# Kernel optimization log

Measured on AMD Instinct MI355X. Metric: run time of the kernel, lower is better.

## Reference

```python
import jax, jax.numpy as jnp
import numpy as np

EPS = 1e-5

def group_norm(x, groups, w, b):
    # x: (B, C, ...) -> normalize over each group of channels + spatial dims
    B, C = x.shape[0], x.shape[1]
    xr = x.reshape(B, groups, -1)
    mu = xr.mean(-1, keepdims=True)
    var = xr.var(-1, keepdims=True)
    xn = ((xr - mu) * jax.lax.rsqrt(var + EPS)).reshape(x.shape)
    wshape = (1, C) + (1,) * (x.ndim - 2)
    return xn * w.reshape(wshape) + b.reshape(wshape)

def dwconv1d(x, w):
    # x: (B, Cg, L), w: (Cg, 1, k) depthwise, 'same' padding (odd k)
    k = w.shape[-1]
    return jax.lax.conv_general_dilated(
        x, w, window_strides=(1,), padding=[(k // 2, k // 2)],
        dimension_numbers=('NCH', 'OIH', 'NCH'),
        feature_group_count=x.shape[1])

def setup_inputs() -> dict:
    key = jax.random.key(0)
    ks = jax.random.split(key, 16)
    B, C, H, W = 32, 256, 56, 56
    Cg = C // 4
    inp = {'x': jax.random.normal(ks[0], (B, C, H, W), jnp.float32)}
    for i, k in enumerate((3, 5, 7, 9)):
        inp[f'dwh{i}'] = jax.random.normal(ks[1 + i], (Cg, 1, k), jnp.float32) * 0.2
        inp[f'dww{i}'] = jax.random.normal(ks[5 + i], (Cg, 1, k), jnp.float32) * 0.2
    inp['gnh_w'] = jnp.ones((C,), jnp.float32)
    inp['gnh_b'] = jnp.zeros((C,), jnp.float32)
    inp['gnw_w'] = jnp.ones((C,), jnp.float32)
    inp['gnw_b'] = jnp.zeros((C,), jnp.float32)
    inp['gn1_w'] = jnp.ones((C,), jnp.float32)
    inp['gn1_b'] = jnp.zeros((C,), jnp.float32)
    inp['wq'] = jax.random.normal(ks[13], (C,), jnp.float32)
    inp['wk'] = jax.random.normal(ks[14], (C,), jnp.float32)
    inp['wv'] = jax.random.normal(ks[15], (C,), jnp.float32)
    return inp

def reference(x, dwh0, dwh1, dwh2, dwh3, dww0, dww1, dww2, dww3,
              gnh_w, gnh_b, gnw_w, gnw_b, gn1_w, gn1_b, wq, wk, wv):
    B, C, H, W = x.shape
    n, Cg, p, gn_groups = 4, C // 4, 7, 4
    dwh = (dwh0, dwh1, dwh2, dwh3)
    dww = (dww0, dww1, dww2, dww3)

    # ---- SMSA: pooled multi-kernel depthwise 1D convs ----
    x_h = x.mean(axis=3)  # (B, C, H)
    x_w = x.mean(axis=2)  # (B, C, W)
    h_cat = jnp.concatenate(
        [dwconv1d(x_h[:, i * Cg:(i + 1) * Cg], dwh[i]) for i in range(n)], axis=1)
    w_cat = jnp.concatenate(
        [dwconv1d(x_w[:, i * Cg:(i + 1) * Cg], dww[i]) for i in range(n)], axis=1)
    Ah = jax.nn.sigmoid(group_norm(h_cat, gn_groups, gnh_w, gnh_b))  # (B,C,H)
    Aw = jax.nn.sigmoid(group_norm(w_cat, gn_groups, gnw_w, gnw_b))  # (B,C,W)
    x_s = x * (Ah[..., :, None] * Aw[..., None, :])  # (B,C,H,W)

    # ---- PCSA: adaptive pool to (p,p) then channel self-attention ----
    # H % p == 0 and W % p == 0, so adaptive avg pool == block mean
    xp = x_s.reshape(B, C, p, H // p, p, W // p).mean(axis=(3, 5))  # (B,C,p,p)
    xp = group_norm(xp, 1, gn1_w, gn1_b)
    N = p * p
    xf = xp.reshape(B, C, N)
    q = xf * wq[None, :, None]  # 1x1 depthwise conv == per-channel scale
    k = xf * wk[None, :, None]
    v = xf * wv[None, :, None]
    attn = jnp.einsum('bcn,bdn->bcd', q, k) / np.sqrt(float(N))
    attn = jax.nn.softmax(attn, axis=-1)
    o = jnp.einsum('bcd,bdn->bcn', attn, v)  # (B,C,N)
    Mc = jax.nn.sigmoid(o.mean(axis=-1))  # (B,C) adaptive avg pool to 1
    return x_s * Mc[:, :, None, None]
```

## Files before the change

kernel.cpp:

```cpp
#include <hip/hip_runtime.h>
#include <math.h>

#define B_  32
#define C_  256
#define H_  56
#define W_  56
#define CG_ 64
#define NG_ 4
#define P_  7
#define N_  49
#define XPP_ 52
#define PLP_ 57
#define PLANE_ (H_*W_)
#define NBC_ (B_*C_)
#define EPS_ 1e-5f

typedef float f4v __attribute__((ext_vector_type(4)));
typedef short s4v __attribute__((ext_vector_type(4)));
typedef short s8v __attribute__((ext_vector_type(8)));
typedef unsigned int uint32;

__device__ __forceinline__ float sig_(float v) { return 1.0f / (1.0f + expf(-v)); }

__device__ __forceinline__ short f2bf_(float f) {
  uint32 u = __builtin_bit_cast(uint32, f);
  u = (u + 0x7FFFu + ((u >> 16) & 1u)) >> 16;
  return (short)u;
}
__device__ __forceinline__ float bf2f_(short s) {
  uint32 u = ((uint32)(unsigned short)s) << 16;
  return __builtin_bit_cast(float, u);
}

__global__ __launch_bounds__(256) void k1_means_bf(const float* __restrict__ x,
                                                   float* __restrict__ xh,
                                                   float* __restrict__ xw,
                                                   short* __restrict__ xbf) {
  __shared__ float pl[H_ * PLP_];
  const int bc = blockIdx.x, t = threadIdx.x;
  const f4v* src = (const f4v*)(x + (size_t)bc * PLANE_);
  s4v* bdst = (s4v*)(xbf + (size_t)bc * PLANE_);
  for (int i = t; i < PLANE_ / 4; i += 256) {
    const f4v v = src[i];
    const int h = i / 14, c4 = i % 14;
    const int base = h * PLP_ + 4 * c4;
    pl[base]     = v.x; pl[base + 1] = v.y;
    pl[base + 2] = v.z; pl[base + 3] = v.w;
    s4v b;
    b.x = f2bf_(v.x); b.y = f2bf_(v.y); b.z = f2bf_(v.z); b.w = f2bf_(v.w);
    bdst[i] = b;
  }
  __syncthreads();
  if (t < H_) {
    float s = 0.f;
    #pragma unroll
    for (int w = 0; w < W_; ++w) s += pl[t * PLP_ + w];
    xh[(size_t)bc * H_ + t] = s * (1.0f / W_);
  } else if (t >= 64 && t < 64 + W_) {
    const int w = t - 64;
    float s = 0.f;
    #pragma unroll
    for (int h = 0; h < H_; ++h) s += pl[h * PLP_ + w];
    xw[(size_t)bc * W_ + w] = s * (1.0f / H_);
  }
}

template<int K>
__device__ __forceinline__ void conv_body(const float* __restrict__ sin_,
                                          const float* __restrict__ swt,
                                          int cc, int l0,
                                          float res[4], float& lsum, float& lsq) {
  constexpr int PAD = K / 2;
  float w[K];
  #pragma unroll
  for (int j = 0; j < K; ++j) w[j] = swt[cc * K + j];
  float win[K + 3];
  #pragma unroll
  for (int jj = 0; jj < K + 3; ++jj) {
    const int idx = l0 - PAD + jj;
    win[jj] = (idx >= 0 && idx < H_) ? sin_[cc * H_ + idx] : 0.f;
  }
  #pragma unroll
  for (int p = 0; p < 4; ++p) {
    float s = 0.f;
    #pragma unroll
    for (int j = 0; j < K; ++j) s += win[p + j] * w[j];
    res[p] = s;
    lsum += s; lsq += s * s;
  }
}

__global__ __launch_bounds__(896) void k2_convgn(
    const float* __restrict__ inh, const float* __restrict__ inw,
    float* __restrict__ Ah, float* __restrict__ Aw,
    const float* __restrict__ h0, const float* __restrict__ h1,
    const float* __restrict__ h2, const float* __restrict__ h3,
    const float* __restrict__ w0, const float* __restrict__ w1,
    const float* __restrict__ w2, const float* __restrict__ w3,
    const float* __restrict__ gnh_w, const float* __restrict__ gnh_b,
    const float* __restrict__ gnw_w, const float* __restrict__ gnw_b) {
  __shared__ __align__(16) float sin_[CG_ * H_];
  __shared__ float swt[CG_ * 9];
  __shared__ float redS[14], redQ[14];
  __shared__ float sMu, sRs;
  const int g = blockIdx.x, b = blockIdx.y, zz = blockIdx.z, t = threadIdx.x;
  const float* in = zz ? inw : inh;
  float* outb = zz ? Aw : Ah;
  const float* wt = zz ? ((g == 0) ? w0 : (g == 1) ? w1 : (g == 2) ? w2 : w3)
                       : ((g == 0) ? h0 : (g == 1) ? h1 : (g == 2) ? h2 : h3);
  const float* gw = zz ? gnw_w : gnh_w;
  const float* gb = zz ? gnw_b : gnh_b;
  const size_t base = ((size_t)b * C_ + (size_t)g * CG_) * H_;
  const int k = 3 + 2 * g;

  ((f4v*)sin_)[t] = ((const f4v*)(in + base))[t];
  if (t < CG_ * k) swt[t] = wt[t];
  __syncthreads();

  const int cc = t / 14, quad = t % 14;
  const int l0 = 4 * quad;
  float res[4];
  float lsum = 0.f, lsq = 0.f;
  if (k == 3)      conv_body<3>(sin_, swt, cc, l0, res, lsum, lsq);
  else if (k == 5) conv_body<5>(sin_, swt, cc, l0, res, lsum, lsq);
  else if (k == 7) conv_body<7>(sin_, swt, cc, l0, res, lsum, lsq);
  else             conv_body<9>(sin_, swt, cc, l0, res, lsum, lsq);

  #pragma unroll
  for (int m = 32; m >= 1; m >>= 1) { lsum += __shfl_xor(lsum, m); lsq += __shfl_xor(lsq, m); }
  if ((t & 63) == 0) { redS[t >> 6] = lsum; redQ[t >> 6] = lsq; }
  __syncthreads();
  if (t == 0) {
    float S = 0.f, Q = 0.f;
    #pragma unroll
    for (int j = 0; j < 14; ++j) { S += redS[j]; Q += redQ[j]; }
    const float mu = S / (float)(CG_ * H_);
    sMu = mu; sRs = rsqrtf(Q / (float)(CG_ * H_) - mu * mu + EPS_);
  }
  __syncthreads();
  const float mu = sMu, rs = sRs;
  const int c = g * CG_ + cc;
  const float gwc = gw[c], gbc = gb[c];
  f4v o;
  o.x = sig_((res[0] - mu) * rs * gwc + gbc);
  o.y = sig_((res[1] - mu) * rs * gwc + gbc);
  o.z = sig_((res[2] - mu) * rs * gwc + gbc);
  o.w = sig_((res[3] - mu) * rs * gwc + gbc);
  ((f4v*)(outb + base))[t] = o;
}

__global__ __launch_bounds__(448) void k3_pool_bf4(const short* __restrict__ xbf,
    const float* __restrict__ Ah, const float* __restrict__ Aw,
    float* __restrict__ xp) {
  const int t = threadIdx.x;
  const int wv = t >> 6;
  const int ln = t & 63;
  const int r  = ln >> 3;
  const int pw = ln & 7;
  const int h  = 8 * wv + r;
  const bool act = (pw < 7);
  #pragma unroll
  for (int c = 0; c < 4; ++c) {
    const int bc = blockIdx.x * 4 + c;
    float s = 0.f;
    if (act) {
      const s8v b = ((const s8v*)(xbf + (size_t)bc * PLANE_))[h * 7 + pw];
      const f4v* aw4 = (const f4v*)(Aw + (size_t)bc * W_);
      const f4v awa = aw4[2 * pw];
      const f4v awb = aw4[2 * pw + 1];
      const float ahh = Ah[(size_t)bc * H_ + h];
      s = (bf2f_(b[0]) * awa.x + bf2f_(b[1]) * awa.y
         + bf2f_(b[2]) * awa.z + bf2f_(b[3]) * awa.w
         + bf2f_(b[4]) * awb.x + bf2f_(b[5]) * awb.y
         + bf2f_(b[6]) * awb.z + bf2f_(b[7]) * awb.w) * ahh;
    }
    s += __shfl_xor(s, 8);
    s += __shfl_xor(s, 16);
    s += __shfl_xor(s, 32);
    if (act && r == 0)
      xp[(size_t)bc * XPP_ + wv * 7 + pw] = s * (1.0f / 64.0f);
    if (wv == 6 && ln >= 56 && ln < 59)
      xp[(size_t)bc * XPP_ + 49 + (ln - 56)] = 0.f;
  }
}

__global__ __launch_bounds__(512) void k4_attn(const float* __restrict__ xp,
    const float* __restrict__ gw, const float* __restrict__ gb,
    const float* __restrict__ wq, const float* __restrict__ wk, const float* __restrict__ wv,
    float* __restrict__ Mc) {
  __shared__ __align__(16) float xn[C_ * XPP_];
  __shared__ float vbar[C_];
  __shared__ float swk[C_];
  __shared__ float redS[8], redQ[8];
  __shared__ float sMu, sRs;
  const int chunk = blockIdx.x, b = blockIdx.y, t = threadIdx.x;
  const f4v* src4 = (const f4v*)(xp + (size_t)b * C_ * XPP_);
  f4v* xn4 = (f4v*)xn;

  float lsum = 0.f, lsq = 0.f;
  for (int i = t; i < C_ * XPP_ / 4; i += 512) {
    const f4v v = src4[i];
    xn4[i] = v;
    lsum += v.x + v.y + v.z + v.w;
    lsq  += v.x * v.x + v.y * v.y + v.z * v.z + v.w * v.w;
  }
  if (t < C_) swk[t] = wk[t];
  #pragma unroll
  for (int m = 32; m >= 1; m >>= 1) { lsum += __shfl_xor(lsum, m); lsq += __shfl_xor(lsq, m); }
  if ((t & 63) == 0) { redS[t >> 6] = lsum; redQ[t >> 6] = lsq; }
  __syncthreads();
  if (t == 0) {
    float S = 0.f, Q = 0.f;
    #pragma unroll
    for (int j = 0; j < 8; ++j) { S += redS[j]; Q += redQ[j]; }
    const float mu = S / (float)(C_ * N_);
    sMu = mu; sRs = rsqrtf(Q / (float)(C_ * N_) - mu * mu + EPS_);
  }
  __syncthreads();
  const float mu = sMu, rs = sRs;
  for (int i = t; i < C_ * XPP_ / 4; i += 512) {
    const int c = i / 13, kk = i - c * 13;
    f4v v = xn4[i];
    v.x = (v.x - mu) * rs * gw[c] + gb[c];
    v.y = (v.y - mu) * rs * gw[c] + gb[c];
    v.z = (v.z - mu) * rs * gw[c] + gb[c];
    v.w = (v.w - mu) * rs * gw[c] + gb[c];
    if (kk == 12) { v.y = 0.f; v.z = 0.f; v.w = 0.f; }
    xn4[i] = v;
  }
  __syncthreads();
  if (t < C_) {
    const f4v* row = (const f4v*)&xn[t * XPP_];
    f4v a = row[0];
    #pragma unroll
    for (int j = 1; j < 13; ++j) a += row[j];
    vbar[t] = wv[t] * (a.x + a.y + a.z + a.w) * (1.0f / N_);
  }
  __syncthreads();

  const int rg = t >> 4, q16 = t & 15;
  const int c0 = chunk * 32 + rg;
  f4v qa[13];
  {
    const f4v* r0 = (const f4v*)&xn[c0 * XPP_];
    #pragma unroll
    for (int j = 0; j < 13; ++j) qa[j] = r0[j];
  }
  const float qs0 = wq[c0] * (1.0f / 7.0f);

  float s0[16], vb[16];
  #pragma unroll
  for (int dd = 0; dd < 16; ++dd) {
    const int d = q16 + 16 * dd;
    const f4v* kb = (const f4v*)&xn[d * XPP_];
    f4v a0 = {0.f, 0.f, 0.f, 0.f};
    #pragma unroll
    for (int j = 0; j < 13; ++j) a0 += qa[j] * kb[j];
    s0[dd] = (a0.x + a0.y + a0.z + a0.w) * qs0 * swk[d];
    vb[dd] = vbar[d];
  }
  float m0 = -INFINITY;
  #pragma unroll
  for (int dd = 0; dd < 16; ++dd) m0 = fmaxf(m0, s0[dd]);
  #pragma unroll
  for (int msk = 1; msk < 16; msk <<= 1) m0 = fmaxf(m0, __shfl_xor(m0, msk, 16));
  float e0 = 0.f, a0 = 0.f;
  #pragma unroll
  for (int dd = 0; dd < 16; ++dd) {
    const float x0 = expf(s0[dd] - m0);
    e0 += x0; a0 += x0 * vb[dd];
  }
  #pragma unroll
  for (int msk = 1; msk < 16; msk <<= 1) {
    e0 += __shfl_xor(e0, msk, 16); a0 += __shfl_xor(a0, msk, 16);
  }
  if (q16 == 0) Mc[(size_t)b * C_ + c0] = sig_(a0 / e0);
}

__global__ __launch_bounds__(448) void k5_out_bf4(const short* __restrict__ xbf,
    const float* __restrict__ Ah, const float* __restrict__ Aw,
    const float* __restrict__ Mc, float* __restrict__ out) {
  const int t = threadIdx.x;
  if (t >= H_ * P_) return;
  const int h = t / P_, pw = t % P_;
  #pragma unroll
  for (int c = 0; c < 4; ++c) {
    const int bc = blockIdx.x * 4 + c;
    const s8v b = ((const s8v*)(xbf + (size_t)bc * PLANE_))[t];
    const f4v* aw4 = (const f4v*)(Aw + (size_t)bc * W_);
    const f4v awa = aw4[2 * pw];
    const f4v awb = aw4[2 * pw + 1];
    const float a = Ah[(size_t)bc * H_ + h] * Mc[bc];
    f4v o1, o2;
    o1.x = bf2f_(b[0]) * a * awa.x; o1.y = bf2f_(b[1]) * a * awa.y;
    o1.z = bf2f_(b[2]) * a * awa.z; o1.w = bf2f_(b[3]) * a * awa.w;
    o2.x = bf2f_(b[4]) * a * awb.x; o2.y = bf2f_(b[5]) * a * awb.y;
    o2.z = bf2f_(b[6]) * a * awb.z; o2.w = bf2f_(b[7]) * a * awb.w;
    f4v* oo = (f4v*)(out + (size_t)bc * PLANE_);
    oo[2 * t]     = o1;
    oo[2 * t + 1] = o2;
  }
}

extern "C" void kernel_launch(void* const* d_in, const int* in_sizes, int n_in,
                              void* d_out, int out_size, void* d_ws, size_t ws_size,
                              hipStream_t stream) {
  const float* x     = (const float*)d_in[0];
  const float* dwh0  = (const float*)d_in[1];
  const float* dww0  = (const float*)d_in[2];
  const float* dwh1  = (const float*)d_in[3];
  const float* dww1  = (const float*)d_in[4];
  const float* dwh2  = (const float*)d_in[5];
  const float* dww2  = (const float*)d_in[6];
  const float* dwh3  = (const float*)d_in[7];
  const float* dww3  = (const float*)d_in[8];
  const float* gnh_w = (const float*)d_in[9];
  const float* gnh_b = (const float*)d_in[10];
  const float* gnw_w = (const float*)d_in[11];
  const float* gnw_b = (const float*)d_in[12];
  const float* gn1_w = (const float*)d_in[13];
  const float* gn1_b = (const float*)d_in[14];
  const float* wq    = (const float*)d_in[15];
  const float* wk    = (const float*)d_in[16];
  const float* wv    = (const float*)d_in[17];
  float* out = (float*)d_out;

  float* ws   = (float*)d_ws;
  float* bufh = ws;
  float* bufw = bufh + (size_t)B_ * C_ * H_;
  float* Ah   = bufw + (size_t)B_ * C_ * W_;
  float* Aw   = Ah   + (size_t)B_ * C_ * H_;
  float* xp   = Aw   + (size_t)B_ * C_ * W_;
  float* Mc   = xp   + (size_t)B_ * C_ * XPP_;
  short* xbf  = (short*)(Mc + (size_t)B_ * C_);

  k1_means_bf<<<NBC_, 256, 0, stream>>>(x, bufh, bufw, xbf);
  k2_convgn<<<dim3(NG_, B_, 2), 896, 0, stream>>>(bufh, bufw, Ah, Aw,
      dwh0, dwh1, dwh2, dwh3, dww0, dww1, dww2, dww3,
      gnh_w, gnh_b, gnw_w, gnw_b);
  k3_pool_bf4<<<NBC_ / 4, 448, 0, stream>>>(xbf, Ah, Aw, xp);
  k4_attn<<<dim3(8, B_), 512, 0, stream>>>(xp, gn1_w, gn1_b, wq, wk, wv, Mc);
  k5_out_bf4<<<NBC_ / 4, 448, 0, stream>>>(xbf, Ah, Aw, Mc, out);
}
```

Measured before the change: 83.01 us.

## Fuse channel attention and output scaling into a single kernel

Merges the attention kernel that computes per-channel gates with the output kernel that rescales the bf16 copy of the input. Each block now computes gates for its 32 channels into shared memory, stages the Ah/Aw tiles in LDS, then streams those 32 channel planes to the output. This removes one launch and the global Mc round trip. The risk is that the bandwidth-heavy output pass now runs on only 256 large-LDS blocks instead of many small ones, which can reduce memory-level parallelism.

```diff
diff --git a/kernel.cpp b/kernel.cpp
--- a/kernel.cpp
+++ b/kernel.cpp
@@ -184,16 +184,22 @@
   }
 }
 
-__global__ __launch_bounds__(512) void k4_attn(const float* __restrict__ xp,
+__global__ __launch_bounds__(512) void k45_attn_out(const float* __restrict__ xp,
+    const short* __restrict__ xbf,
+    const float* __restrict__ Ah, const float* __restrict__ Aw,
     const float* __restrict__ gw, const float* __restrict__ gb,
     const float* __restrict__ wq, const float* __restrict__ wk, const float* __restrict__ wv,
-    float* __restrict__ Mc) {
+    float* __restrict__ out) {
   __shared__ __align__(16) float xn[C_ * XPP_];
   __shared__ float vbar[C_];
   __shared__ float swk[C_];
+  __shared__ __align__(16) float sAh[32 * H_];
+  __shared__ __align__(16) float sAw[32 * W_];
+  __shared__ float sMc[32];
   __shared__ float redS[8], redQ[8];
   __shared__ float sMu, sRs;
   const int chunk = blockIdx.x, b = blockIdx.y, t = threadIdx.x;
+  const int cbase = b * C_ + chunk * 32;
   const f4v* src4 = (const f4v*)(xp + (size_t)b * C_ * XPP_);
   f4v* xn4 = (f4v*)xn;
 
@@ -204,6 +210,10 @@
     lsum += v.x + v.y + v.z + v.w;
     lsq  += v.x * v.x + v.y * v.y + v.z * v.z + v.w * v.w;
   }
+  for (int i = t; i < 32 * H_; i += 512)
+    sAh[i] = Ah[(size_t)(cbase + i / H_) * H_ + (i % H_)];
+  for (int i = t; i < 32 * W_; i += 512)
+    sAw[i] = Aw[(size_t)(cbase + i / W_) * W_ + (i % W_)];
   if (t < C_) swk[t] = wk[t];
   #pragma unroll
   for (int m = 32; m >= 1; m >>= 1) { lsum += __shfl_xor(lsum, m); lsq += __shfl_xor(lsq, m); }
@@ -238,67 +248,63 @@
   }
   __syncthreads();
 
-  const int rg = t >> 4, q16 = t & 15;
-  const int c0 = chunk * 32 + rg;
-  f4v qa[13];
   {
-    const f4v* r0 = (const f4v*)&xn[c0 * XPP_];
-    #pragma unroll
-    for (int j = 0; j < 13; ++j) qa[j] = r0[j];
-  }
-  const float qs0 = wq[c0] * (1.0f / 7.0f);
-
-  float s0[16], vb[16];
-  #pragma unroll
-  for (int dd = 0; dd < 16; ++dd) {
-    const int d = q16 + 16 * dd;
-    const f4v* kb = (const f4v*)&xn[d * XPP_];
-    f4v a0 = {0.f, 0.f, 0.f, 0.f};
-    #pragma unroll
-    for (int j = 0; j < 13; ++j) a0 += qa[j] * kb[j];
-    s0[dd] = (a0.x + a0.y + a0.z + a0.w) * qs0 * swk[d];
-    vb[dd] = vbar[d];
-  }
-  float m0 = -INFINITY;
-  #pragma unroll
-  for (int dd = 0; dd < 16; ++dd) m0 = fmaxf(m0, s0[dd]);
-  #pragma unroll
-  for (int msk = 1; msk < 16; msk <<= 1) m0 = fmaxf(m0, __shfl_xor(m0, msk, 16));
-  float e0 = 0.f, a0 = 0.f;
-  #pragma unroll
-  for (int dd = 0; dd < 16; ++dd) {
-    const float x0 = expf(s0[dd] - m0);
-    e0 += x0; a0 += x0 * vb[dd];
-  }
-  #pragma unroll
-  for (int msk = 1; msk < 16; msk <<= 1) {
-    e0 += __shfl_xor(e0, msk, 16); a0 += __shfl_xor(a0, msk, 16);
-  }
-  if (q16 == 0) Mc[(size_t)b * C_ + c0] = sig_(a0 / e0);
-}
-
-__global__ __launch_bounds__(448) void k5_out_bf4(const short* __restrict__ xbf,
-    const float* __restrict__ Ah, const float* __restrict__ Aw,
-    const float* __restrict__ Mc, float* __restrict__ out) {
-  const int t = threadIdx.x;
-  if (t >= H_ * P_) return;
-  const int h = t / P_, pw = t % P_;
-  #pragma unroll
-  for (int c = 0; c < 4; ++c) {
-    const int bc = blockIdx.x * 4 + c;
-    const s8v b = ((const s8v*)(xbf + (size_t)bc * PLANE_))[t];
-    const f4v* aw4 = (const f4v*)(Aw + (size_t)bc * W_);
-    const f4v awa = aw4[2 * pw];
-    const f4v awb = aw4[2 * pw + 1];
-    const float a = Ah[(size_t)bc * H_ + h] * Mc[bc];
+    const int rg = t >> 4, q16 = t & 15;
+    const int c0 = chunk * 32 + rg;
+    f4v qa[13];
+    {
+      const f4v* r0 = (const f4v*)&xn[c0 * XPP_];
+      #pragma unroll
+      for (int j = 0; j < 13; ++j) qa[j] = r0[j];
+    }
+    const float qs0 = wq[c0] * (1.0f / 7.0f);
+    float s0[16], vb[16];
+    #pragma unroll
+    for (int dd = 0; dd < 16; ++dd) {
+      const int d = q16 + 16 * dd;
+      const f4v* kb = (const f4v*)&xn[d * XPP_];
+      f4v a0 = {0.f, 0.f, 0.f, 0.f};
+      #pragma unroll
+      for (int j = 0; j < 13; ++j) a0 += qa[j] * kb[j];
+      s0[dd] = (a0.x + a0.y + a0.z + a0.w) * qs0 * swk[d];
+      vb[dd] = vbar[d];
+    }
+    float m0 = -INFINITY;
+    #pragma unroll
+    for (int dd = 0; dd < 16; ++dd) m0 = fmaxf(m0, s0[dd]);
+    #pragma unroll
+    for (int msk = 1; msk < 16; msk <<= 1) m0 = fmaxf(m0, __shfl_xor(m0, msk, 16));
+    float e0 = 0.f, a0 = 0.f;
+    #pragma unroll
+    for (int dd = 0; dd < 16; ++dd) {
+      const float x0 = expf(s0[dd] - m0);
+      e0 += x0; a0 += x0 * vb[dd];
+    }
+    #pragma unroll
+    for (int msk = 1; msk < 16; msk <<= 1) {
+      e0 += __shfl_xor(e0, msk, 16); a0 += __shfl_xor(a0, msk, 16);
+    }
+    if (q16 == 0) sMc[rg] = sig_(a0 / e0);
+  }
+  __syncthreads();
+
+  const s8v* xx = (const s8v*)(xbf + (size_t)cbase * PLANE_);
+  f4v* oo = (f4v*)(out + (size_t)cbase * PLANE_);
+  const f4v* sAw4 = (const f4v*)sAw;
+  for (int i = t; i < 32 * 392; i += 512) {
+    const int cc = i / 392, j2 = i - cc * 392;
+    const int h = j2 / 7, pw = j2 - h * 7;
+    const s8v bb = xx[i];
+    const float a = sAh[cc * H_ + h] * sMc[cc];
+    const f4v awa = sAw4[cc * 14 + 2 * pw];
+    const f4v awb = sAw4[cc * 14 + 2 * pw + 1];
     f4v o1, o2;
-    o1.x = bf2f_(b[0]) * a * awa.x; o1.y = bf2f_(b[1]) * a * awa.y;
-    o1.z = bf2f_(b[2]) * a * awa.z; o1.w = bf2f_(b[3]) * a * awa.w;
-    o2.x = bf2f_(b[4]) * a * awb.x; o2.y = bf2f_(b[5]) * a * awb.y;
-    o2.z = bf2f_(b[6]) * a * awb.z; o2.w = bf2f_(b[7]) * a * awb.w;
-    f4v* oo = (f4v*)(out + (size_t)bc * PLANE_);
-    oo[2 * t]     = o1;
-    oo[2 * t + 1] = o2;
+    o1.x = bf2f_(bb[0]) * a * awa.x; o1.y = bf2f_(bb[1]) * a * awa.y;
+    o1.z = bf2f_(bb[2]) * a * awa.z; o1.w = bf2f_(bb[3]) * a * awa.w;
+    o2.x = bf2f_(bb[4]) * a * awb.x; o2.y = bf2f_(bb[5]) * a * awb.y;
+    o2.z = bf2f_(bb[6]) * a * awb.z; o2.w = bf2f_(bb[7]) * a * awb.w;
+    oo[2 * i]     = o1;
+    oo[2 * i + 1] = o2;
   }
 }
 
@@ -331,14 +337,13 @@
   float* Ah   = bufw + (size_t)B_ * C_ * W_;
   float* Aw   = Ah   + (size_t)B_ * C_ * H_;
   float* xp   = Aw   + (size_t)B_ * C_ * W_;
-  float* Mc   = xp   + (size_t)B_ * C_ * XPP_;
-  short* xbf  = (short*)(Mc + (size_t)B_ * C_);
+  short* xbf  = (short*)(xp + (size_t)B_ * C_ * XPP_);
 
   k1_means_bf<<<NBC_, 256, 0, stream>>>(x, bufh, bufw, xbf);
   k2_convgn<<<dim3(NG_, B_, 2), 896, 0, stream>>>(bufh, bufw, Ah, Aw,
       dwh0, dwh1, dwh2, dwh3, dww0, dww1, dww2, dww3,
       gnh_w, gnh_b, gnw_w, gnw_b);
   k3_pool_bf4<<<NBC_ / 4, 448, 0, stream>>>(xbf, Ah, Aw, xp);
-  k4_attn<<<dim3(8, B_), 512, 0, stream>>>(xp, gn1_w, gn1_b, wq, wk, wv, Mc);
-  k5_out_bf4<<<NBC_ / 4, 448, 0, stream>>>(xbf, Ah, Aw, Mc, out);
-}
+  k45_attn_out<<<dim3(8, B_), 512, 0, stream>>>(xp, xbf, Ah, Aw,
+      gn1_w, gn1_b, wq, wk, wv, out);
+}
```

New measurement: 83.76 us. No clear change (+0.9%).
